# Kernel optimization log

Measured on AMD Instinct MI355X. Metric: run time of the kernel, lower is better.

The kernel has to match this reference:

```python
import jax, jax.numpy as jnp
import numpy as np

EMBED = 1024
HEADS = 16
HEAD_DIM = EMBED // HEADS
OUT_DIM = 1024


def setup_inputs() -> dict:
    key = jax.random.key(0)
    ks = jax.random.split(key, 8)
    N, L = 2, 2048
    values = jax.random.normal(ks[0], (N, L, EMBED), dtype=jnp.float32)
    keys_t = jax.random.normal(ks[1], (N, L, EMBED), dtype=jnp.float32)
    query = jax.random.normal(ks[2], (N, L, EMBED), dtype=jnp.float32)
    s = 1.0 / np.sqrt(HEAD_DIM)
    Wv = jax.random.normal(ks[3], (HEAD_DIM, HEAD_DIM), dtype=jnp.float32) * s
    Wk = jax.random.normal(ks[4], (HEAD_DIM, HEAD_DIM), dtype=jnp.float32) * s
    Wq = jax.random.normal(ks[5], (HEAD_DIM, HEAD_DIM), dtype=jnp.float32) * s
    Wout = jax.random.normal(ks[6], (OUT_DIM, EMBED), dtype=jnp.float32) * (1.0 / np.sqrt(EMBED))
    bout = jax.random.normal(ks[7], (OUT_DIM,), dtype=jnp.float32) * 0.01
    return {"values": values, "keys": keys_t, "query": query,
            "Wv": Wv, "Wk": Wk, "Wq": Wq, "Wout": Wout, "bout": bout}


def reference(values, keys, query, Wv, Wk, Wq, Wout, bout):
    N, Lq, _ = query.shape
    Lk = keys.shape[1]
    # split into heads: (N, L, H, D)
    v = values.reshape(N, Lk, HEADS, HEAD_DIM)
    k = keys.reshape(N, Lk, HEADS, HEAD_DIM)
    q = query.reshape(N, Lq, HEADS, HEAD_DIM)
    # per-head shared linear projections (torch Linear: x @ W.T, no bias)
    v = jnp.einsum('nlhd,ed->nlhe', v, Wv)
    k = jnp.einsum('nlhd,ed->nlhe', k, Wk)
    q = jnp.einsum('nqhd,ed->nqhe', q, Wq)
    # scores (N, H, Q, K); NOTE: scale is 1/sqrt(embed_size), per original code
    scores = jnp.einsum('nqhd,nkhd->nhqk', q, k) / jnp.sqrt(jnp.float32(EMBED))
    attn = jax.nn.softmax(scores, axis=-1)
    out = jnp.einsum('nhqk,nkhd->nqhd', attn, v).reshape(N, Lq, EMBED)
    # fc_out: x @ Wout.T + bout
    return out @ Wout.T + bout
```

## Files before the change

### kernel.cpp

```cpp
#include <hip/hip_runtime.h>
#include <cstdint>

typedef __attribute__((ext_vector_type(8))) short short8;
typedef __attribute__((ext_vector_type(4))) float floatx4;

#define DEV __device__ __forceinline__

constexpr int NB = 2, Lseq = 2048, NH = 16, HD = 64, EMB = 1024;
constexpr float QSCALE = 0.03125f * 1.4426950408889634f;

DEV uint16_t f2bf(float f) {
  uint32_t x = __builtin_bit_cast(uint32_t, f);
  x += 0x7fffu + ((x >> 16) & 1u);
  return (uint16_t)(x >> 16);
}

DEV uint32_t pack2(float lo, float hi) {
  uint32_t a = __builtin_bit_cast(uint32_t, lo) + 0x8000u;
  uint32_t b = __builtin_bit_cast(uint32_t, hi) + 0x8000u;
  return __builtin_amdgcn_perm(b, a, 0x07060302);
}

DEV void gl_lds16(const void* g, void* l) {
  __builtin_amdgcn_global_load_lds((const __attribute__((address_space(1))) void*)g,
                                   (__attribute__((address_space(3))) void*)l, 16, 0, 0);
}

DEV short8 ld8bf(const float* p, float sc) {
  float4 u = *(const float4*)p;
  float4 v = *(const float4*)(p + 4);
  union { short8 s; uint32_t d[4]; } r;
  r.d[0] = pack2(u.x * sc, u.y * sc);
  r.d[1] = pack2(u.z * sc, u.w * sc);
  r.d[2] = pack2(v.x * sc, v.y * sc);
  r.d[3] = pack2(v.z * sc, v.w * sc);
  return r.s;
}

__global__ __launch_bounds__(256) void prep_kernel(
    const float* __restrict__ values, const float* __restrict__ keysrc,
    const float* __restrict__ query, const float* __restrict__ Wv,
    const float* __restrict__ Wk, const float* __restrict__ Wq,
    const float* __restrict__ Wout,
    uint16_t* __restrict__ qp, uint16_t* __restrict__ kp,
    uint16_t* __restrict__ vp, uint16_t* __restrict__ wbf) {
  const int t = threadIdx.x, w = t >> 6, lane = t & 63;
  const int quad = lane >> 4, l16 = lane & 15;
  const int wid = blockIdx.x * 4 + w;
  const int mat = wid >> 10, sub = wid & 1023;

  if (mat == 3) {
#pragma unroll
    for (int i = 0; i < 4; ++i) {
      int idx = sub * 256 + i * 64 + lane;
      float4 v = ((const float4*)Wout)[idx];
      uint2 p;
      p.x = pack2(v.x, v.y);
      p.y = pack2(v.z, v.w);
      ((uint2*)wbf)[idx] = p;
    }
    return;
  }

  floatx4 c[4][4];
#pragma unroll
  for (int i = 0; i < 4; ++i)
#pragma unroll
    for (int j = 0; j < 4; ++j) c[i][j] = floatx4{0.f, 0.f, 0.f, 0.f};

  if (mat < 2) {
    const float* src = mat ? keysrc : query;
    const float* W   = mat ? Wk : Wq;
    const float bsc  = mat ? 1.f : QSCALE;
    uint16_t* dst    = mat ? kp : qp;
    const int R0 = sub * 64;
    short8 a[4][2], b[4][2];
#pragma unroll
    for (int dc = 0; dc < 2; ++dc) {
#pragma unroll
      for (int f = 0; f < 4; ++f) {
        a[f][dc] = ld8bf(src + (size_t)(R0 + f * 16 + l16) * 64 + dc * 32 + quad * 8, 1.f);
        b[f][dc] = ld8bf(W + (size_t)(f * 16 + l16) * 64 + dc * 32 + quad * 8, bsc);
      }
    }
#pragma unroll
    for (int dc = 0; dc < 2; ++dc)
#pragma unroll
      for (int mf = 0; mf < 4; ++mf)
#pragma unroll
        for (int nf = 0; nf < 4; ++nf)
          c[mf][nf] = __builtin_amdgcn_mfma_f32_16x16x32_bf16(a[mf][dc], b[nf][dc], c[mf][nf], 0, 0, 0);
#pragma unroll
    for (int mf = 0; mf < 4; ++mf) {
#pragma unroll
      for (int rr = 0; rr < 4; ++rr) {
        int r = R0 + mf * 16 + quad * 4 + rr;
        int h = r & 15, l = (r >> 4) & 2047, n = r >> 15;
        uint16_t* drow = dst + ((size_t)(n * 16 + h) * 2048 + l) * 64;
#pragma unroll
        for (int nf = 0; nf < 4; ++nf) drow[nf * 16 + l16] = f2bf(c[mf][nf][rr]);
      }
    }
  } else {
    const int nh = sub >> 5, L0 = (sub & 31) * 64;
    const int n = nh >> 4, h = nh & 15;
    short8 a[4][2], b[4][2];
#pragma unroll
    for (int dc = 0; dc < 2; ++dc) {
#pragma unroll
      for (int f = 0; f < 4; ++f) {
        a[f][dc] = ld8bf(Wv + (size_t)(f * 16 + l16) * 64 + dc * 32 + quad * 8, 1.f);
        b[f][dc] = ld8bf(values + (size_t)(n * 2048 + L0 + f * 16 + l16) * 1024 + h * 64 + dc * 32 + quad * 8, 1.f);
      }
    }
#pragma unroll
    for (int dc = 0; dc < 2; ++dc)
#pragma unroll
      for (int mf = 0; mf < 4; ++mf)
#pragma unroll
        for (int nf = 0; nf < 4; ++nf)
          c[mf][nf] = __builtin_amdgcn_mfma_f32_16x16x32_bf16(a[mf][dc], b[nf][dc], c[mf][nf], 0, 0, 0);
#pragma unroll
    for (int mf = 0; mf < 4; ++mf) {
#pragma unroll
      for (int rr = 0; rr < 4; ++rr) {
        int d = mf * 16 + quad * 4 + rr;
        uint16_t* drow = vp + ((size_t)nh * 64 + d) * 2048 + L0;
#pragma unroll
        for (int nf = 0; nf < 4; ++nf) drow[nf * 16 + l16] = f2bf(c[mf][nf][rr]);
      }
    }
  }
}

__global__ __launch_bounds__(256) void flash_kernel(const uint16_t* __restrict__ qp,
                                                    const uint16_t* __restrict__ kp,
                                                    const uint16_t* __restrict__ vp,
                                                    uint16_t* __restrict__ xatt) {
  __shared__ uint16_t Kt[2][64 * 64];
  __shared__ uint16_t Vt[2][64 * 64];
  __shared__ uint16_t Pt[4][32 * 72];
  const int t = threadIdx.x;
  const int w = t >> 6, lane = t & 63, quad = lane >> 4, l16 = lane & 15;
  const int nh = blockIdx.y;
  const int q0 = blockIdx.x * 128 + w * 32;
  const uint16_t* Qb = qp + (size_t)nh * Lseq * HD;
  const uint16_t* Kb = kp + (size_t)nh * Lseq * HD;
  const uint16_t* Vb = vp + (size_t)nh * HD * Lseq;
  const int srow = lane >> 3, sc8 = (lane & 7) ^ (lane >> 3);

  short8 bq[2][2];
#pragma unroll
  for (int qb = 0; qb < 2; ++qb) {
    bq[qb][0] = *(const short8*)(Qb + (q0 + qb * 16 + l16) * 64 + quad * 8);
    bq[qb][1] = *(const short8*)(Qb + (q0 + qb * 16 + l16) * 64 + 32 + quad * 8);
  }

  floatx4 o[4][2];
  float psum[2] = {0.f, 0.f};
#pragma unroll
  for (int i = 0; i < 4; ++i)
#pragma unroll
    for (int qb = 0; qb < 2; ++qb) o[i][qb] = floatx4{0.f, 0.f, 0.f, 0.f};

#pragma unroll
  for (int i = 0; i < 2; ++i) {
    int r0 = w * 16 + i * 8;
    gl_lds16(Kb + (r0 + srow) * 64 + sc8 * 8, &Kt[0][r0 * 64]);
    gl_lds16(Vb + (size_t)(r0 + srow) * Lseq + sc8 * 8, &Vt[0][r0 * 64]);
  }

  for (int kb = 0; kb < Lseq / 64; ++kb) {
    __syncthreads();
    const int cur = kb & 1;
    if (kb + 1 < Lseq / 64) {
      const int nxt = cur ^ 1;
      const uint16_t* kg = Kb + (kb + 1) * (64 * 64);
#pragma unroll
      for (int i = 0; i < 2; ++i) {
        int r0 = w * 16 + i * 8;
        gl_lds16(kg + (r0 + srow) * 64 + sc8 * 8, &Kt[nxt][r0 * 64]);
        gl_lds16(Vb + (size_t)(r0 + srow) * Lseq + (kb + 1) * 64 + sc8 * 8, &Vt[nxt][r0 * 64]);
      }
    }

    floatx4 s[4][2];
#pragma unroll
    for (int kb16 = 0; kb16 < 4; ++kb16)
#pragma unroll
      for (int qb = 0; qb < 2; ++qb) s[kb16][qb] = floatx4{0.f, 0.f, 0.f, 0.f};
#pragma unroll
    for (int dc = 0; dc < 2; ++dc) {
#pragma unroll
      for (int kb16 = 0; kb16 < 4; ++kb16) {
        int row = kb16 * 16 + l16;
        short8 ak = *(const short8*)(&Kt[cur][row * 64 + ((dc * 4 + quad) ^ (row & 7)) * 8]);
        s[kb16][0] = __builtin_amdgcn_mfma_f32_16x16x32_bf16(ak, bq[0][dc], s[kb16][0], 0, 0, 0);
        s[kb16][1] = __builtin_amdgcn_mfma_f32_16x16x32_bf16(ak, bq[1][dc], s[kb16][1], 0, 0, 0);
      }
    }

#pragma unroll
    for (int qb = 0; qb < 2; ++qb) {
      uint16_t* pw = &Pt[w][(qb * 16 + l16) * 72];
#pragma unroll
      for (int kb16 = 0; kb16 < 4; ++kb16) {
        float p0 = __builtin_amdgcn_exp2f(s[kb16][qb][0]);
        float p1 = __builtin_amdgcn_exp2f(s[kb16][qb][1]);
        float p2 = __builtin_amdgcn_exp2f(s[kb16][qb][2]);
        float p3 = __builtin_amdgcn_exp2f(s[kb16][qb][3]);
        psum[qb] += (p0 + p1) + (p2 + p3);
        uint2 pk;
        pk.x = pack2(p0, p1);
        pk.y = pack2(p2, p3);
        *(uint2*)(pw + kb16 * 16 + quad * 4) = pk;
      }
    }

    short8 bp[2][2];
#pragma unroll
    for (int qb = 0; qb < 2; ++qb)
#pragma unroll
      for (int kc = 0; kc < 2; ++kc)
        bp[qb][kc] = *(const short8*)(&Pt[w][(qb * 16 + l16) * 72 + kc * 32 + quad * 8]);
#pragma unroll
    for (int kc = 0; kc < 2; ++kc) {
#pragma unroll
      for (int db = 0; db < 4; ++db) {
        int row = db * 16 + l16;
        short8 av = *(const short8*)(&Vt[cur][row * 64 + ((kc * 4 + quad) ^ (row & 7)) * 8]);
        o[db][0] = __builtin_amdgcn_mfma_f32_16x16x32_bf16(av, bp[0][kc], o[db][0], 0, 0, 0);
        o[db][1] = __builtin_amdgcn_mfma_f32_16x16x32_bf16(av, bp[1][kc], o[db][1], 0, 0, 0);
      }
    }
  }

  const int n = nh >> 4, h = nh & 15;
#pragma unroll
  for (int qb = 0; qb < 2; ++qb) {
    float l = psum[qb];
    l += __shfl_xor(l, 16, 64);
    l += __shfl_xor(l, 32, 64);
    float inv = 1.f / l;
    size_t rowb = (size_t)(n * Lseq + q0 + qb * 16 + l16) * EMB + h * 64;
#pragma unroll
    for (int db = 0; db < 4; ++db) {
      uint2 pk;
      pk.x = pack2(o[db][qb][0] * inv, o[db][qb][1] * inv);
      pk.y = pack2(o[db][qb][2] * inv, o[db][qb][3] * inv);
      *(uint2*)(xatt + rowb + db * 16 + quad * 4) = pk;
    }
  }
}

__global__ __launch_bounds__(256) void gemm_out_kernel(const uint16_t* __restrict__ X,
                                                       const uint16_t* __restrict__ Wb,
                                                       const float* __restrict__ bias,
                                                       float* __restrict__ out) {
  __shared__ uint16_t Xt[2][128 * 64];
  __shared__ uint16_t Wt[2][64 * 64];
  const int t = threadIdx.x, w = t >> 6, lane = t & 63, quad = lane >> 4, l16 = lane & 15;
  const int m0 = blockIdx.x * 128, o0 = blockIdx.y * 64;
  const int srow = lane >> 3, sc8 = (lane & 7) ^ (lane >> 3);
  floatx4 c[2][4];
#pragma unroll
  for (int i = 0; i < 2; ++i)
#pragma unroll
    for (int j = 0; j < 4; ++j) c[i][j] = floatx4{0.f, 0.f, 0.f, 0.f};

#pragma unroll
  for (int i = 0; i < 4; ++i) {
    int r0 = w * 32 + i * 8;
    gl_lds16(X + (size_t)(m0 + r0 + srow) * 1024 + sc8 * 8, &Xt[0][r0 * 64]);
  }
#pragma unroll
  for (int i = 0; i < 2; ++i) {
    int r0 = w * 16 + i * 8;
    gl_lds16(Wb + (size_t)(o0 + r0 + srow) * 1024 + sc8 * 8, &Wt[0][r0 * 64]);
  }

  for (int kt = 0; kt < 16; ++kt) {
    __syncthreads();
    const int cur = kt & 1;
    if (kt + 1 < 16) {
      const int nxt = cur ^ 1;
      const int e0 = (kt + 1) * 64;
#pragma unroll
      for (int i = 0; i < 4; ++i) {
        int r0 = w * 32 + i * 8;
        gl_lds16(X + (size_t)(m0 + r0 + srow) * 1024 + e0 + sc8 * 8, &Xt[nxt][r0 * 64]);
      }
#pragma unroll
      for (int i = 0; i < 2; ++i) {
        int r0 = w * 16 + i * 8;
        gl_lds16(Wb + (size_t)(o0 + r0 + srow) * 1024 + e0 + sc8 * 8, &Wt[nxt][r0 * 64]);
      }
    }
#pragma unroll
    for (int kc = 0; kc < 2; ++kc) {
      short8 a[2], b[4];
#pragma unroll
      for (int mf = 0; mf < 2; ++mf) {
        int row = w * 32 + mf * 16 + l16;
        a[mf] = *(const short8*)(&Xt[cur][row * 64 + ((kc * 4 + quad) ^ (row & 7)) * 8]);
      }
#pragma unroll
      for (int nf = 0; nf < 4; ++nf) {
        int rw = nf * 16 + l16;
        b[nf] = *(const short8*)(&Wt[cur][rw * 64 + ((kc * 4 + quad) ^ (rw & 7)) * 8]);
      }
#pragma unroll
      for (int mf = 0; mf < 2; ++mf)
#pragma unroll
        for (int nf = 0; nf < 4; ++nf)
          c[mf][nf] = __builtin_amdgcn_mfma_f32_16x16x32_bf16(a[mf], b[nf], c[mf][nf], 0, 0, 0);
    }
  }
#pragma unroll
  for (int nf = 0; nf < 4; ++nf) {
    float bv = bias[o0 + nf * 16 + l16];
#pragma unroll
    for (int mf = 0; mf < 2; ++mf)
#pragma unroll
      for (int r = 0; r < 4; ++r)
        out[(size_t)(m0 + w * 32 + mf * 16 + quad * 4 + r) * 1024 + o0 + nf * 16 + l16] =
            c[mf][nf][r] + bv;
  }
}

extern "C" void kernel_launch(void* const* d_in, const int* in_sizes, int n_in,
                              void* d_out, int out_size, void* d_ws, size_t ws_size,
                              hipStream_t stream) {
  const float* values = (const float*)d_in[0];
  const float* keys   = (const float*)d_in[1];
  const float* query  = (const float*)d_in[2];
  const float* Wv     = (const float*)d_in[3];
  const float* Wk     = (const float*)d_in[4];
  const float* Wq     = (const float*)d_in[5];
  const float* Wout   = (const float*)d_in[6];
  const float* bout   = (const float*)d_in[7];
  float* out = (float*)d_out;

  uint16_t* ws  = (uint16_t*)d_ws;
  uint16_t* qp  = ws;
  uint16_t* kp  = ws + (size_t)4194304;
  uint16_t* vp  = ws + (size_t)2 * 4194304;
  uint16_t* xat = ws + (size_t)3 * 4194304;
  uint16_t* wbf = ws + (size_t)4 * 4194304;

  prep_kernel<<<dim3(1024), dim3(256), 0, stream>>>(values, keys, query, Wv, Wk, Wq, Wout,
                                                    qp, kp, vp, wbf);
  flash_kernel<<<dim3(16, 32), dim3(256), 0, stream>>>(qp, kp, vp, xat);
  gemm_out_kernel<<<dim3(32, 16), dim3(256), 0, stream>>>(xat, wbf, bout, out);
}
```

Measured before the change: 187.4 us.

## Split flash attention over two key halves and combine partials

Flash attention is split along the key dimension into two halves via a third grid dimension, doubling the block count from 512 to 1024 to better fill the GPU's compute units. Each half writes unnormalized fp32 partial outputs and row sums to workspace, and a new combine kernel adds them, normalizes, and writes the bf16 attention output. The split path needs extra workspace, adds a kernel launch and fp32 partial traffic, and runs only when the workspace is large enough. The output GEMM grid is also transposed so consecutive blocks walk output columns for a fixed row tile.

```diff
diff --git a/kernel.cpp b/kernel.cpp
--- a/kernel.cpp
+++ b/kernel.cpp
@@ -136,17 +136,21 @@
 __global__ __launch_bounds__(256) void flash_kernel(const uint16_t* __restrict__ qp,
                                                     const uint16_t* __restrict__ kp,
                                                     const uint16_t* __restrict__ vp,
-                                                    uint16_t* __restrict__ xatt) {
+                                                    uint16_t* __restrict__ xatt,
+                                                    float* __restrict__ opart,
+                                                    float* __restrict__ psum_g,
+                                                    int kbn) {
   __shared__ uint16_t Kt[2][64 * 64];
   __shared__ uint16_t Vt[2][64 * 64];
   __shared__ uint16_t Pt[4][32 * 72];
   const int t = threadIdx.x;
   const int w = t >> 6, lane = t & 63, quad = lane >> 4, l16 = lane & 15;
-  const int nh = blockIdx.y;
-  const int q0 = blockIdx.x * 128 + w * 32;
+  const int nh = blockIdx.y, qt = blockIdx.x, kh = blockIdx.z;
+  const int q0 = qt * 128 + w * 32;
   const uint16_t* Qb = qp + (size_t)nh * Lseq * HD;
-  const uint16_t* Kb = kp + (size_t)nh * Lseq * HD;
+  const uint16_t* Kb = kp + (size_t)nh * Lseq * HD + (size_t)kh * kbn * 64 * 64;
   const uint16_t* Vb = vp + (size_t)nh * HD * Lseq;
+  const int vcol0 = kh * kbn * 64;
   const int srow = lane >> 3, sc8 = (lane & 7) ^ (lane >> 3);
 
   short8 bq[2][2];
@@ -167,20 +171,20 @@
   for (int i = 0; i < 2; ++i) {
     int r0 = w * 16 + i * 8;
     gl_lds16(Kb + (r0 + srow) * 64 + sc8 * 8, &Kt[0][r0 * 64]);
-    gl_lds16(Vb + (size_t)(r0 + srow) * Lseq + sc8 * 8, &Vt[0][r0 * 64]);
-  }
-
-  for (int kb = 0; kb < Lseq / 64; ++kb) {
+    gl_lds16(Vb + (size_t)(r0 + srow) * Lseq + vcol0 + sc8 * 8, &Vt[0][r0 * 64]);
+  }
+
+  for (int kb = 0; kb < kbn; ++kb) {
     __syncthreads();
     const int cur = kb & 1;
-    if (kb + 1 < Lseq / 64) {
+    if (kb + 1 < kbn) {
       const int nxt = cur ^ 1;
       const uint16_t* kg = Kb + (kb + 1) * (64 * 64);
 #pragma unroll
       for (int i = 0; i < 2; ++i) {
         int r0 = w * 16 + i * 8;
         gl_lds16(kg + (r0 + srow) * 64 + sc8 * 8, &Kt[nxt][r0 * 64]);
-        gl_lds16(Vb + (size_t)(r0 + srow) * Lseq + (kb + 1) * 64 + sc8 * 8, &Vt[nxt][r0 * 64]);
+        gl_lds16(Vb + (size_t)(r0 + srow) * Lseq + vcol0 + (kb + 1) * 64 + sc8 * 8, &Vt[nxt][r0 * 64]);
       }
     }
 
@@ -235,22 +239,72 @@
     }
   }
 
+  if (opart) {
+    float* ob = opart + (((size_t)nh * 16 + qt) * 2 + kh) * 8192 + (size_t)w * 8 * 256;
+#pragma unroll
+    for (int db = 0; db < 4; ++db)
+#pragma unroll
+      for (int qb = 0; qb < 2; ++qb)
+        *(floatx4*)(ob + (db * 2 + qb) * 256 + lane * 4) = o[db][qb];
+#pragma unroll
+    for (int qb = 0; qb < 2; ++qb) {
+      float l = psum[qb];
+      l += __shfl_xor(l, 16, 64);
+      l += __shfl_xor(l, 32, 64);
+      if (quad == 0)
+        psum_g[(((size_t)nh * 16 + qt) * 2 + kh) * 128 + w * 32 + qb * 16 + l16] = l;
+    }
+  } else {
+    const int n = nh >> 4, h = nh & 15;
+#pragma unroll
+    for (int qb = 0; qb < 2; ++qb) {
+      float l = psum[qb];
+      l += __shfl_xor(l, 16, 64);
+      l += __shfl_xor(l, 32, 64);
+      float inv = 1.f / l;
+      size_t rowb = (size_t)(n * Lseq + q0 + qb * 16 + l16) * EMB + h * 64;
+#pragma unroll
+      for (int db = 0; db < 4; ++db) {
+        uint2 pk;
+        pk.x = pack2(o[db][qb][0] * inv, o[db][qb][1] * inv);
+        pk.y = pack2(o[db][qb][2] * inv, o[db][qb][3] * inv);
+        *(uint2*)(xatt + rowb + db * 16 + quad * 4) = pk;
+      }
+    }
+  }
+}
+
+__global__ __launch_bounds__(256) void combine_kernel(const float* __restrict__ opart,
+                                                      const float* __restrict__ psum_g,
+                                                      uint16_t* __restrict__ xatt) {
+  const int t = threadIdx.x, w = t >> 6, lane = t & 63, quad = lane >> 4, l16 = lane & 15;
+  const int qt = blockIdx.x, nh = blockIdx.y;
   const int n = nh >> 4, h = nh & 15;
+  const size_t tb = ((size_t)nh * 16 + qt) * 2;
+  const float* oa = opart + tb * 8192 + (size_t)w * 8 * 256;
+  const float* ob = opart + (tb + 1) * 8192 + (size_t)w * 8 * 256;
+  float inv[2];
 #pragma unroll
   for (int qb = 0; qb < 2; ++qb) {
-    float l = psum[qb];
-    l += __shfl_xor(l, 16, 64);
-    l += __shfl_xor(l, 32, 64);
-    float inv = 1.f / l;
-    size_t rowb = (size_t)(n * Lseq + q0 + qb * 16 + l16) * EMB + h * 64;
-#pragma unroll
-    for (int db = 0; db < 4; ++db) {
+    int q = w * 32 + qb * 16 + l16;
+    inv[qb] = 1.f / (psum_g[tb * 128 + q] + psum_g[(tb + 1) * 128 + q]);
+  }
+#pragma unroll
+  for (int db = 0; db < 4; ++db)
+#pragma unroll
+    for (int qb = 0; qb < 2; ++qb) {
+      floatx4 a = *(const floatx4*)(oa + (db * 2 + qb) * 256 + lane * 4);
+      floatx4 b = *(const floatx4*)(ob + (db * 2 + qb) * 256 + lane * 4);
+      float v0 = (a[0] + b[0]) * inv[qb];
+      float v1 = (a[1] + b[1]) * inv[qb];
+      float v2 = (a[2] + b[2]) * inv[qb];
+      float v3 = (a[3] + b[3]) * inv[qb];
       uint2 pk;
-      pk.x = pack2(o[db][qb][0] * inv, o[db][qb][1] * inv);
-      pk.y = pack2(o[db][qb][2] * inv, o[db][qb][3] * inv);
-      *(uint2*)(xatt + rowb + db * 16 + quad * 4) = pk;
-    }
-  }
+      pk.x = pack2(v0, v1);
+      pk.y = pack2(v2, v3);
+      size_t row = (size_t)(n * Lseq + qt * 128 + w * 32 + qb * 16 + l16) * EMB + h * 64;
+      *(uint2*)(xatt + row + db * 16 + quad * 4) = pk;
+    }
 }
 
 __global__ __launch_bounds__(256) void gemm_out_kernel(const uint16_t* __restrict__ X,
@@ -260,7 +314,7 @@
   __shared__ uint16_t Xt[2][128 * 64];
   __shared__ uint16_t Wt[2][64 * 64];
   const int t = threadIdx.x, w = t >> 6, lane = t & 63, quad = lane >> 4, l16 = lane & 15;
-  const int m0 = blockIdx.x * 128, o0 = blockIdx.y * 64;
+  const int m0 = blockIdx.y * 128, o0 = blockIdx.x * 64;
   const int srow = lane >> 3, sc8 = (lane & 7) ^ (lane >> 3);
   floatx4 c[2][4];
 #pragma unroll
@@ -347,9 +401,17 @@
   uint16_t* vp  = ws + (size_t)2 * 4194304;
   uint16_t* xat = ws + (size_t)3 * 4194304;
   uint16_t* wbf = ws + (size_t)4 * 4194304;
+  float* opart  = (float*)(ws + (size_t)17825792);
+  float* psum   = opart + (size_t)8388608;
+  const bool split = ws_size >= 69730304ull;
 
   prep_kernel<<<dim3(1024), dim3(256), 0, stream>>>(values, keys, query, Wv, Wk, Wq, Wout,
                                                     qp, kp, vp, wbf);
-  flash_kernel<<<dim3(16, 32), dim3(256), 0, stream>>>(qp, kp, vp, xat);
-  gemm_out_kernel<<<dim3(32, 16), dim3(256), 0, stream>>>(xat, wbf, bout, out);
-}
+  if (split) {
+    flash_kernel<<<dim3(16, 32, 2), dim3(256), 0, stream>>>(qp, kp, vp, nullptr, opart, psum, 16);
+    combine_kernel<<<dim3(16, 32), dim3(256), 0, stream>>>(opart, psum, xat);
+  } else {
+    flash_kernel<<<dim3(16, 32, 1), dim3(256), 0, stream>>>(qp, kp, vp, xat, nullptr, nullptr, 32);
+  }
+  gemm_out_kernel<<<dim3(16, 32), dim3(256), 0, stream>>>(xat, wbf, bout, out);
+}
```

After: 188.0 us. No clear change (+0.3%).
